# Optimization experiments

Hardware: AMD Instinct MI355X
Metric: run time of the kernel (lower is better)

The kernel has to match this reference:

```python
import jax, jax.numpy as jnp
import numpy as np

B, T, D = 4, 2048, 1024
DEPTH = 4
LEAF_DIM = 256
NUM_LEAVES = 2 ** DEPTH          # 16
NUM_NODES = NUM_LEAVES - 1       # 15


def _uniform(key, shape, scale):
    s = 1.0 / np.sqrt(scale)
    return jax.random.uniform(key, shape, minval=-s, maxval=s, dtype=jnp.float32)


def setup_inputs() -> dict:
    key = jax.random.key(0)
    ks = jax.random.split(key, 8)
    x = jax.random.normal(ks[0], (B, T, D), dtype=jnp.float32)
    # gate params: Dense(1) per internal node, level-order layout
    node_w = _uniform(ks[1], (NUM_NODES, D), D)
    node_b = _uniform(ks[2], (NUM_NODES,), D)
    # leaf MLP params: D -> LEAF_DIM -> D, stacked over leaves
    w1 = _uniform(ks[3], (NUM_LEAVES, D, LEAF_DIM), D)
    b1 = _uniform(ks[4], (NUM_LEAVES, LEAF_DIM), D)
    w2 = _uniform(ks[5], (NUM_LEAVES, LEAF_DIM, D), LEAF_DIM)
    b2 = _uniform(ks[6], (NUM_LEAVES, D), LEAF_DIM)
    return {"x": x, "node_w": node_w, "node_b": node_b,
            "w1": w1, "b1": b1, "w2": w2, "b2": b2, "training": 0}


def _leaf_probs(x, node_w, node_b, depth):
    # gate activations for all internal nodes at once: [B,T,NUM_NODES]
    c = jax.nn.sigmoid(jnp.einsum('btd,nd->btn', x, node_w) + node_b)
    probs = jnp.ones(c.shape[:-1] + (1,), dtype=c.dtype)
    for m in range(depth):
        start = 2 ** m - 1
        cl = c[..., start:start + 2 ** m]          # gates at level m: [B,T,2^m]
        # left child gets c, right child gets (1-c); interleave preserves
        # the recursion's n -> (2n, 2n+1) indexing
        probs = jnp.stack([probs * cl, probs * (1.0 - cl)], axis=-1)
        probs = probs.reshape(probs.shape[:-2] + (-1,))
    return probs                                   # [B,T,NUM_LEAVES]


def reference(x, node_w, node_b, w1, b1, w2, b2, training):
    num_leaves = w1.shape[0]
    depth = int(np.log2(num_leaves))
    probs = _leaf_probs(x, node_w, node_b, depth)          # [B,T,L]
    # all leaf MLP hidden layers as one batched GEMM
    h = jax.nn.relu(jnp.einsum('btd,ldh->btlh', x, w1) + b1)
    # weight hidden by leaf probability, then contract l and h together so the
    # [B,T,L,D] per-leaf output is never materialized
    h = h * probs[..., None]
    out = jnp.einsum('btlh,lhd->btd', h, w2)
    out = out + jnp.einsum('btl,ld->btd', probs, b2)
    return out
```

## Files before the change

kernel.cpp:

```cpp
#include <hip/hip_runtime.h>
#include <stdint.h>

typedef unsigned short ushort_t;
typedef __bf16 bf16x8 __attribute__((ext_vector_type(8)));
typedef float f32x4 __attribute__((ext_vector_type(4)));

#define M_TOK 8192
#define K1 1024
#define N1 4096
#define K2 4160
#define N2 1024

template <int V> struct ic { static constexpr int value = V; };

__device__ __forceinline__ ushort_t f2bf(float f) {
  union { float f; unsigned u; } v; v.f = f;
  unsigned u = v.u;
  u += 0x7FFFu + ((u >> 16) & 1u);
  return (ushort_t)(u >> 16);
}

__device__ __forceinline__ void gload16(const void* g, void* l) {
  __builtin_amdgcn_global_load_lds((__attribute__((address_space(1))) void*)g,
                                   (__attribute__((address_space(3))) void*)l,
                                   16, 0, 0);
}

__global__ __launch_bounds__(256) void k_prep(
    const float* __restrict__ x, const float* __restrict__ node_w,
    const float* __restrict__ node_b, const float* __restrict__ w1,
    const float* __restrict__ w2, const float* __restrict__ b2,
    ushort_t* __restrict__ xb, float* __restrict__ probs,
    ushort_t* __restrict__ w1t, ushort_t* __restrict__ w2t,
    ushort_t* __restrict__ hp) {
  __shared__ ushort_t tile[64][68];
  const int b = blockIdx.x;
  if (b < 1024) {
    const int tr = threadIdx.x >> 4, tc = (threadIdx.x & 15) * 4;
    const int l = b >> 6, rem = b & 63;
    const int kt = rem >> 2, ht = rem & 3;
    const float* in = w1 + (size_t)l * K1 * 256;
#pragma unroll
    for (int rr = 0; rr < 4; ++rr) {
      int r = tr + rr * 16;
      float4 v = *(const float4*)(in + (size_t)(kt * 64 + r) * 256 + ht * 64 + tc);
      tile[r][tc+0] = f2bf(v.x); tile[r][tc+1] = f2bf(v.y);
      tile[r][tc+2] = f2bf(v.z); tile[r][tc+3] = f2bf(v.w);
    }
    __syncthreads();
#pragma unroll
    for (int rr = 0; rr < 4; ++rr) {
      int oh = tr + rr * 16;
      ushort4 o;
      o.x = tile[tc+0][oh]; o.y = tile[tc+1][oh];
      o.z = tile[tc+2][oh]; o.w = tile[tc+3][oh];
      *(ushort4*)(w1t + (size_t)(l * 256 + ht * 64 + oh) * K1 + kt * 64 + tc) = o;
    }
  } else if (b < 2048) {
    const int tr = threadIdx.x >> 4, tc = (threadIdx.x & 15) * 4;
    const int bb = b - 1024;
    const int l = bb >> 6, rem = bb & 63;
    const int ht = rem >> 4, dt = rem & 15;
    const float* in = w2 + (size_t)l * 256 * N2;
#pragma unroll
    for (int rr = 0; rr < 4; ++rr) {
      int r = tr + rr * 16;
      float4 v = *(const float4*)(in + (size_t)(ht * 64 + r) * N2 + dt * 64 + tc);
      tile[r][tc+0] = f2bf(v.x); tile[r][tc+1] = f2bf(v.y);
      tile[r][tc+2] = f2bf(v.z); tile[r][tc+3] = f2bf(v.w);
    }
    __syncthreads();
#pragma unroll
    for (int rr = 0; rr < 4; ++rr) {
      int od = tr + rr * 16;
      ushort4 o;
      o.x = tile[tc+0][od]; o.y = tile[tc+1][od];
      o.z = tile[tc+2][od]; o.w = tile[tc+3][od];
      *(ushort4*)(w2t + (size_t)(dt * 64 + od) * K2 + l * 256 + ht * 64 + tc) = o;
    }
  } else if (b < 2304) {
    int tid = (b - 2048) * 256 + threadIdx.x;
    int d = tid >> 6, cc = tid & 63;
    float v = (cc < 16) ? b2[cc * N2 + d] : 0.f;
    w2t[(size_t)d * K2 + 4096 + cc] = f2bf(v);
  } else {
    const int wid = threadIdx.x >> 6, lane = threadIdx.x & 63;
    const int t = (b - 2304) * 4 + wid;
    const float* xr = x + (size_t)t * K1;
    float xv[16];
#pragma unroll
    for (int j = 0; j < 4; ++j) {
      float4 v = *(const float4*)(xr + j * 256 + lane * 4);
      xv[4*j+0] = v.x; xv[4*j+1] = v.y; xv[4*j+2] = v.z; xv[4*j+3] = v.w;
    }
    ushort_t* xbr = xb + (size_t)t * K1;
#pragma unroll
    for (int j = 0; j < 4; ++j) {
      ushort4 o;
      o.x = f2bf(xv[4*j+0]); o.y = f2bf(xv[4*j+1]);
      o.z = f2bf(xv[4*j+2]); o.w = f2bf(xv[4*j+3]);
      *(ushort4*)(xbr + j * 256 + lane * 4) = o;
    }
    float c[15];
#pragma unroll
    for (int n = 0; n < 15; ++n) {
      float s = 0.f;
      const float* wr = node_w + n * K1;
#pragma unroll
      for (int j = 0; j < 4; ++j) {
        float4 w = *(const float4*)(wr + j * 256 + lane * 4);
        s += xv[4*j+0]*w.x + xv[4*j+1]*w.y + xv[4*j+2]*w.z + xv[4*j+3]*w.w;
      }
#pragma unroll
      for (int off = 32; off > 0; off >>= 1) s += __shfl_xor(s, off);
      float z = s + node_b[n];
      c[n] = 1.f / (1.f + __expf(-z));
    }
    if (lane < 16) {
      float p = 1.f;
#pragma unroll
      for (int m = 0; m < 4; ++m) {
        int jm = lane >> (4 - m);
        int node = (1 << m) - 1 + jm;
        int bit = (lane >> (3 - m)) & 1;
        p *= bit ? (1.f - c[node]) : c[node];
      }
      probs[t * 16 + lane] = p;
      hp[(size_t)t * K2 + 4096 + lane] = f2bf(p);
    }
    if (lane < 48) hp[(size_t)t * K2 + 4112 + lane] = 0;
  }
}

template <int NT, int LDA, int LDB, int BN, int MODE>
__global__ __launch_bounds__(512, 2) void k_gemm8(
    const ushort_t* __restrict__ A, const ushort_t* __restrict__ Bt,
    const float* __restrict__ probs, const float* __restrict__ b1,
    ushort_t* __restrict__ hp, float* __restrict__ out, int ntn) {
  constexpr int BHR = BN / 2;
  constexpr int WN = (BN == 256) ? 4 : 2;
  constexpr int WM = 8 / WN;
  constexpr int FH = 128 / (WM * 16);
  constexpr int ABYTES = 128 * 128;
  constexpr int BBYTES = BHR * 128;
  constexpr int KEEP = 2 + 2 * (BHR / 64);

  extern __shared__ char lds[];
  const int tid = threadIdx.x;
  int bid = blockIdx.x;
  const int nwg = gridDim.x;
  bid = (bid & 7) * (nwg >> 3) + (bid >> 3);
  const int bm = bid / ntn, bn = bid % ntn;

  const int wid = tid >> 6, lane = tid & 63;
  const int widM = wid / WN, widN = wid % WN;
  const int wmBase = widM * (FH * 16);
  const int wn = widN * 64;
  const int lr = lane & 15, g = lane >> 4;

  const ushort_t* Ag = A + (size_t)bm * 256 * LDA;
  const ushort_t* Bg = Bt + (size_t)bn * BN * LDB;

  const int srow = tid >> 3;
  const int scol = ((tid & 7) << 4) ^ ((srow & 7) << 4);

  const char* pA = (const char*)(Ag + (size_t)srow * LDA) + scol;
  const char* pB = (const char*)(Bg + (size_t)srow * LDB) + scol;

  auto stageA = [&](int buf, int half, int kt) {
    const char* src = pA + (size_t)(half * 128) * (LDA * 2) + kt * 128;
    char* dst = lds + (buf * 2 + half) * ABYTES + tid * 16;
#pragma unroll
    for (int r = 0; r < 2; ++r)
      gload16(src + (size_t)(r * 64) * (LDA * 2), dst + r * 8192);
  };
  auto stageB = [&](int buf, int half, int kt) {
    const char* src = pB + (size_t)(half * BHR) * (LDB * 2) + kt * 128;
    char* dst = lds + 4 * ABYTES + (buf * 2 + half) * BBYTES + tid * 16;
#pragma unroll
    for (int r = 0; r < BHR / 64; ++r)
      gload16(src + (size_t)(r * 64) * (LDB * 2), dst + r * 8192);
  };
  auto rdA = [&](int buf, int half, int i, int kk) -> bf16x8 {
    int r = wmBase + i * 16 + lr;
    int off = r * 128 + (((kk * 4 + g) ^ (lr & 7)) << 4);
    return *(const bf16x8*)(lds + (buf * 2 + half) * ABYTES + off);
  };
  auto rdB = [&](int buf, int j, int kk) -> bf16x8 {
    int nr = wn + j * 16;
    int half = (nr >= BHR) ? 1 : 0;
    int r = (nr & (BHR - 1)) + lr;
    int off = r * 128 + (((kk * 4 + g) ^ (lr & 7)) << 4);
    return *(const bf16x8*)(lds + 4 * ABYTES + (buf * 2 + half) * BBYTES + off);
  };

  f32x4 acc[2 * FH][4];
#pragma unroll
  for (int i = 0; i < 2 * FH; ++i)
#pragma unroll
    for (int j = 0; j < 4; ++j) acc[i][j] = (f32x4){0.f, 0.f, 0.f, 0.f};

  stageA(0, 0, 0); stageA(0, 1, 0); stageB(0, 0, 0); stageB(0, 1, 0);
  stageA(1, 0, 1); stageB(1, 0, 1); stageB(1, 1, 1);
  if constexpr (KEEP == 6) asm volatile("s_waitcnt vmcnt(6)" ::: "memory");
  else                     asm volatile("s_waitcnt vmcnt(4)" ::: "memory");
  __builtin_amdgcn_sched_barrier(0);
  __builtin_amdgcn_s_barrier();
  __builtin_amdgcn_sched_barrier(0);

  auto body = [&](auto CURC, int kt) {
    constexpr int cur = decltype(CURC)::value;
    bf16x8 bfr[2][4];
    {
      bf16x8 a0[FH][2];
#pragma unroll
      for (int kk = 0; kk < 2; ++kk) {
#pragma unroll
        for (int i = 0; i < FH; ++i) a0[i][kk] = rdA(cur, 0, i, kk);
#pragma unroll
        for (int j = 0; j < 4; ++j) bfr[kk][j] = rdB(cur, j, kk);
      }
      if (kt + 1 < NT) stageA(cur ^ 1, 1, kt + 1);
      __builtin_amdgcn_s_setprio(1);
#pragma unroll
      for (int kk = 0; kk < 2; ++kk)
#pragma unroll
        for (int j = 0; j < 4; ++j)
#pragma unroll
          for (int i = 0; i < FH; ++i)
            acc[i][j] = __builtin_amdgcn_mfma_f32_16x16x32_bf16(
                a0[i][kk], bfr[kk][j], acc[i][j], 0, 0, 0);
      __builtin_amdgcn_s_setprio(0);
    }
    __builtin_amdgcn_s_barrier();
    __builtin_amdgcn_sched_barrier(0);
    {
      bf16x8 a1[FH][2];
#pragma unroll
      for (int kk = 0; kk < 2; ++kk)
#pragma unroll
        for (int i = 0; i < FH; ++i) a1[i][kk] = rdA(cur, 1, i, kk);
      if (kt + 2 < NT) {
        stageA(cur, 0, kt + 2);
        stageB(cur, 0, kt + 2);
        stageB(cur, 1, kt + 2);
      }
      __builtin_amdgcn_s_setprio(1);
#pragma unroll
      for (int kk = 0; kk < 2; ++kk)
#pragma unroll
        for (int j = 0; j < 4; ++j)
#pragma unroll
          for (int i = 0; i < FH; ++i)
            acc[FH + i][j] = __builtin_amdgcn_mfma_f32_16x16x32_bf16(
                a1[i][kk], bfr[kk][j], acc[FH + i][j], 0, 0, 0);
      __builtin_amdgcn_s_setprio(0);
    }
    if (kt + 2 < NT) {
      if constexpr (KEEP == 6) asm volatile("s_waitcnt vmcnt(6)" ::: "memory");
      else                     asm volatile("s_waitcnt vmcnt(4)" ::: "memory");
      __builtin_amdgcn_sched_barrier(0);
    } else if (kt + 1 < NT) {
      asm volatile("s_waitcnt vmcnt(0)" ::: "memory");
      __builtin_amdgcn_sched_barrier(0);
    }
    __builtin_amdgcn_s_barrier();
    __builtin_amdgcn_sched_barrier(0);
  };

  int kt = 0;
#pragma unroll 1
  for (int it = 0; it < NT / 2; ++it) {
    body(ic<0>{}, kt); ++kt;
    body(ic<1>{}, kt); ++kt;
  }
  if constexpr (NT & 1) body(ic<0>{}, kt);

  const int rowb = bm * 256 + wmBase + g * 4;
  const int colb = bn * BN + wn + lr;
  if (MODE == 0) {
    const int leaf = bn;
#pragma unroll
    for (int q = 0; q < 2; ++q)
#pragma unroll
      for (int i = 0; i < FH; ++i) {
        int rbase = rowb + q * 128 + i * 16;
        float pm[4];
#pragma unroll
        for (int rg = 0; rg < 4; ++rg)
          pm[rg] = probs[(size_t)(rbase + rg) * 16 + leaf];
#pragma unroll
        for (int j = 0; j < 4; ++j) {
          float bias = b1[colb + j * 16];
#pragma unroll
          for (int rg = 0; rg < 4; ++rg) {
            float v = acc[q * FH + i][j][rg] + bias;
            v = v > 0.f ? v : 0.f;
            v *= pm[rg];
            hp[(size_t)(rbase + rg) * K2 + colb + j * 16] = f2bf(v);
          }
        }
      }
  } else {
#pragma unroll
    for (int q = 0; q < 2; ++q)
#pragma unroll
      for (int i = 0; i < FH; ++i) {
        int rbase = rowb + q * 128 + i * 16;
#pragma unroll
        for (int j = 0; j < 4; ++j)
#pragma unroll
          for (int rg = 0; rg < 4; ++rg)
            out[(size_t)(rbase + rg) * N2 + colb + j * 16] = acc[q * FH + i][j][rg];
      }
  }
}

extern "C" void kernel_launch(void* const* d_in, const int* in_sizes, int n_in,
                              void* d_out, int out_size, void* d_ws, size_t ws_size,
                              hipStream_t stream) {
  const float* x      = (const float*)d_in[0];
  const float* node_w = (const float*)d_in[1];
  const float* node_b = (const float*)d_in[2];
  const float* w1     = (const float*)d_in[3];
  const float* b1     = (const float*)d_in[4];
  const float* w2     = (const float*)d_in[5];
  const float* b2     = (const float*)d_in[6];
  float* out = (float*)d_out;

  char* ws = (char*)d_ws;
  ushort_t* xb    = (ushort_t*)(ws);
  ushort_t* w1t   = (ushort_t*)(ws + 16777216);
  ushort_t* w2t   = (ushort_t*)(ws + 25165824);
  ushort_t* hp    = (ushort_t*)(ws + 33685504);
  float*    probs = (float*)   (ws + 101842944);

  k_prep<<<4352, 256, 0, stream>>>(x, node_w, node_b, w1, w2, b2,
                                   xb, probs, w1t, w2t, hp);
  k_gemm8<16, K1, K1, 256, 0><<<512, 512, 131072, stream>>>(
      xb, w1t, probs, b1, hp, nullptr, N1 / 256);
  k_gemm8<65, K2, K2, 128, 1><<<256, 512, 98304, stream>>>(
      hp, w2t, nullptr, nullptr, nullptr, out, N2 / 128);
}
```

Measured before the change: 169.0 us.

## Shrink GEMM tiles to 128 rows and K-step 32 for higher occupancy

The templated GEMM now uses a BM=128 row tile and a 32-element K step per stage, down from 256 rows and 64. Each single A buffer is loaded whole instead of in two halves, and the LDS swizzle is redone for 64-byte rows. LDS use drops to 48KB and 32KB per block, launch bounds allow 4 blocks per CU, and the grids double. Occupancy and wave count go up to hide latency better, at the cost of twice as many K iterations and barriers, less data reuse per tile and more global traffic.

```diff
diff --git a/kernel.cpp b/kernel.cpp
--- a/kernel.cpp
+++ b/kernel.cpp
@@ -132,18 +132,21 @@
   }
 }
 
-template <int NT, int LDA, int LDB, int BN, int MODE>
-__global__ __launch_bounds__(512, 2) void k_gemm8(
+template <int NT, int LDA, int LDB, int BM, int BN, int THREADS, int MODE>
+__global__ __launch_bounds__(THREADS, 4) void k_gemm(
     const ushort_t* __restrict__ A, const ushort_t* __restrict__ Bt,
     const float* __restrict__ probs, const float* __restrict__ b1,
     ushort_t* __restrict__ hp, float* __restrict__ out, int ntn) {
+  constexpr int NWAVE = THREADS / 64;
+  constexpr int WN = (BN == 256) ? 4 : 2;
+  constexpr int WM = NWAVE / WN;
+  constexpr int HA = BM / 2;
+  constexpr int FH = HA / (WM * 16);
   constexpr int BHR = BN / 2;
-  constexpr int WN = (BN == 256) ? 4 : 2;
-  constexpr int WM = 8 / WN;
-  constexpr int FH = 128 / (WM * 16);
-  constexpr int ABYTES = 128 * 128;
-  constexpr int BBYTES = BHR * 128;
-  constexpr int KEEP = 2 + 2 * (BHR / 64);
+  constexpr int ATILE = BM * 64;
+  constexpr int BBYTES = BHR * 64;
+  constexpr int BOFF = 2 * ATILE;
+  constexpr int AR = (BM * 64) / (THREADS * 16);
 
   extern __shared__ char lds[];
   const int tid = threadIdx.x;
@@ -157,41 +160,35 @@
   const int wmBase = widM * (FH * 16);
   const int wn = widN * 64;
   const int lr = lane & 15, g = lane >> 4;
-
-  const ushort_t* Ag = A + (size_t)bm * 256 * LDA;
+  const int swz = (g ^ ((lr >> 1) & 3)) << 4;
+
+  const ushort_t* Ag = A + (size_t)bm * BM * LDA;
   const ushort_t* Bg = Bt + (size_t)bn * BN * LDB;
 
-  const int srow = tid >> 3;
-  const int scol = ((tid & 7) << 4) ^ ((srow & 7) << 4);
-
-  const char* pA = (const char*)(Ag + (size_t)srow * LDA) + scol;
-  const char* pB = (const char*)(Bg + (size_t)srow * LDB) + scol;
-
-  auto stageA = [&](int buf, int half, int kt) {
-    const char* src = pA + (size_t)(half * 128) * (LDA * 2) + kt * 128;
-    char* dst = lds + (buf * 2 + half) * ABYTES + tid * 16;
-#pragma unroll
-    for (int r = 0; r < 2; ++r)
-      gload16(src + (size_t)(r * 64) * (LDA * 2), dst + r * 8192);
+  auto stageA = [&](int buf, int kt) {
+#pragma unroll
+    for (int r = 0; r < AR; ++r) {
+      int srow = (tid >> 2) + r * (THREADS / 4);
+      int scol = (((tid & 3) ^ ((srow >> 1) & 3)) << 4);
+      gload16((const char*)(Ag + (size_t)srow * LDA) + kt * 64 + scol,
+              lds + buf * ATILE + r * (THREADS * 16) + tid * 16);
+    }
   };
   auto stageB = [&](int buf, int half, int kt) {
-    const char* src = pB + (size_t)(half * BHR) * (LDB * 2) + kt * 128;
-    char* dst = lds + 4 * ABYTES + (buf * 2 + half) * BBYTES + tid * 16;
-#pragma unroll
-    for (int r = 0; r < BHR / 64; ++r)
-      gload16(src + (size_t)(r * 64) * (LDB * 2), dst + r * 8192);
-  };
-  auto rdA = [&](int buf, int half, int i, int kk) -> bf16x8 {
-    int r = wmBase + i * 16 + lr;
-    int off = r * 128 + (((kk * 4 + g) ^ (lr & 7)) << 4);
-    return *(const bf16x8*)(lds + (buf * 2 + half) * ABYTES + off);
-  };
-  auto rdB = [&](int buf, int j, int kk) -> bf16x8 {
+    int srow = tid >> 2;
+    int scol = (((tid & 3) ^ ((srow >> 1) & 3)) << 4);
+    gload16((const char*)(Bg + (size_t)(half * BHR + srow) * LDB) + kt * 64 + scol,
+            lds + BOFF + (buf * 2 + half) * BBYTES + tid * 16);
+  };
+  auto rdA = [&](int buf, int half, int i) -> bf16x8 {
+    int row = half * HA + wmBase + i * 16 + lr;
+    return *(const bf16x8*)(lds + buf * ATILE + row * 64 + swz);
+  };
+  auto rdB = [&](int buf, int j) -> bf16x8 {
     int nr = wn + j * 16;
     int half = (nr >= BHR) ? 1 : 0;
     int r = (nr & (BHR - 1)) + lr;
-    int off = r * 128 + (((kk * 4 + g) ^ (lr & 7)) << 4);
-    return *(const bf16x8*)(lds + 4 * ABYTES + (buf * 2 + half) * BBYTES + off);
+    return *(const bf16x8*)(lds + BOFF + (buf * 2 + half) * BBYTES + r * 64 + swz);
   };
 
   f32x4 acc[2 * FH][4];
@@ -200,65 +197,50 @@
 #pragma unroll
     for (int j = 0; j < 4; ++j) acc[i][j] = (f32x4){0.f, 0.f, 0.f, 0.f};
 
-  stageA(0, 0, 0); stageA(0, 1, 0); stageB(0, 0, 0); stageB(0, 1, 0);
-  stageA(1, 0, 1); stageB(1, 0, 1); stageB(1, 1, 1);
-  if constexpr (KEEP == 6) asm volatile("s_waitcnt vmcnt(6)" ::: "memory");
-  else                     asm volatile("s_waitcnt vmcnt(4)" ::: "memory");
+  stageA(0, 0); stageB(0, 0, 0); stageB(0, 1, 0);
+  stageB(1, 0, 1); stageB(1, 1, 1);
+  asm volatile("s_waitcnt vmcnt(2)" ::: "memory");
   __builtin_amdgcn_sched_barrier(0);
   __builtin_amdgcn_s_barrier();
   __builtin_amdgcn_sched_barrier(0);
 
   auto body = [&](auto CURC, int kt) {
     constexpr int cur = decltype(CURC)::value;
-    bf16x8 bfr[2][4];
+    bf16x8 bfr[4];
     {
-      bf16x8 a0[FH][2];
-#pragma unroll
-      for (int kk = 0; kk < 2; ++kk) {
-#pragma unroll
-        for (int i = 0; i < FH; ++i) a0[i][kk] = rdA(cur, 0, i, kk);
-#pragma unroll
-        for (int j = 0; j < 4; ++j) bfr[kk][j] = rdB(cur, j, kk);
-      }
-      if (kt + 1 < NT) stageA(cur ^ 1, 1, kt + 1);
+      bf16x8 a0[FH];
+#pragma unroll
+      for (int i = 0; i < FH; ++i) a0[i] = rdA(cur, 0, i);
+#pragma unroll
+      for (int j = 0; j < 4; ++j) bfr[j] = rdB(cur, j);
+      if (kt + 1 < NT) stageA(cur ^ 1, kt + 1);
       __builtin_amdgcn_s_setprio(1);
 #pragma unroll
-      for (int kk = 0; kk < 2; ++kk)
-#pragma unroll
-        for (int j = 0; j < 4; ++j)
-#pragma unroll
-          for (int i = 0; i < FH; ++i)
-            acc[i][j] = __builtin_amdgcn_mfma_f32_16x16x32_bf16(
-                a0[i][kk], bfr[kk][j], acc[i][j], 0, 0, 0);
+      for (int j = 0; j < 4; ++j)
+#pragma unroll
+        for (int i = 0; i < FH; ++i)
+          acc[i][j] = __builtin_amdgcn_mfma_f32_16x16x32_bf16(
+              a0[i], bfr[j], acc[i][j], 0, 0, 0);
       __builtin_amdgcn_s_setprio(0);
     }
     __builtin_amdgcn_s_barrier();
     __builtin_amdgcn_sched_barrier(0);
     {
-      bf16x8 a1[FH][2];
-#pragma unroll
-      for (int kk = 0; kk < 2; ++kk)
-#pragma unroll
-        for (int i = 0; i < FH; ++i) a1[i][kk] = rdA(cur, 1, i, kk);
-      if (kt + 2 < NT) {
-        stageA(cur, 0, kt + 2);
-        stageB(cur, 0, kt + 2);
-        stageB(cur, 1, kt + 2);
-      }
+      bf16x8 a1[FH];
+#pragma unroll
+      for (int i = 0; i < FH; ++i) a1[i] = rdA(cur, 1, i);
+      if (kt + 2 < NT) { stageB(cur, 0, kt + 2); stageB(cur, 1, kt + 2); }
       __builtin_amdgcn_s_setprio(1);
 #pragma unroll
-      for (int kk = 0; kk < 2; ++kk)
-#pragma unroll
-        for (int j = 0; j < 4; ++j)
-#pragma unroll
-          for (int i = 0; i < FH; ++i)
-            acc[FH + i][j] = __builtin_amdgcn_mfma_f32_16x16x32_bf16(
-                a1[i][kk], bfr[kk][j], acc[FH + i][j], 0, 0, 0);
+      for (int j = 0; j < 4; ++j)
+#pragma unroll
+        for (int i = 0; i < FH; ++i)
+          acc[FH + i][j] = __builtin_amdgcn_mfma_f32_16x16x32_bf16(
+              a1[i], bfr[j], acc[FH + i][j], 0, 0, 0);
       __builtin_amdgcn_s_setprio(0);
     }
     if (kt + 2 < NT) {
-      if constexpr (KEEP == 6) asm volatile("s_waitcnt vmcnt(6)" ::: "memory");
-      else                     asm volatile("s_waitcnt vmcnt(4)" ::: "memory");
+      asm volatile("s_waitcnt vmcnt(2)" ::: "memory");
       __builtin_amdgcn_sched_barrier(0);
     } else if (kt + 1 < NT) {
       asm volatile("s_waitcnt vmcnt(0)" ::: "memory");
@@ -274,9 +256,8 @@
     body(ic<0>{}, kt); ++kt;
     body(ic<1>{}, kt); ++kt;
   }
-  if constexpr (NT & 1) body(ic<0>{}, kt);
-
-  const int rowb = bm * 256 + wmBase + g * 4;
+
+  const int rowb = bm * BM + wmBase + g * 4;
   const int colb = bn * BN + wn + lr;
   if (MODE == 0) {
     const int leaf = bn;
@@ -284,7 +265,7 @@
     for (int q = 0; q < 2; ++q)
 #pragma unroll
       for (int i = 0; i < FH; ++i) {
-        int rbase = rowb + q * 128 + i * 16;
+        int rbase = rowb + q * HA + i * 16;
         float pm[4];
 #pragma unroll
         for (int rg = 0; rg < 4; ++rg)
@@ -306,7 +287,7 @@
     for (int q = 0; q < 2; ++q)
 #pragma unroll
       for (int i = 0; i < FH; ++i) {
-        int rbase = rowb + q * 128 + i * 16;
+        int rbase = rowb + q * HA + i * 16;
 #pragma unroll
         for (int j = 0; j < 4; ++j)
 #pragma unroll
@@ -337,8 +318,8 @@
 
   k_prep<<<4352, 256, 0, stream>>>(x, node_w, node_b, w1, w2, b2,
                                    xb, probs, w1t, w2t, hp);
-  k_gemm8<16, K1, K1, 256, 0><<<512, 512, 131072, stream>>>(
+  k_gemm<32, K1, K1, 128, 256, 512, 0><<<1024, 512, 49152, stream>>>(
       xb, w1t, probs, b1, hp, nullptr, N1 / 256);
-  k_gemm8<65, K2, K2, 128, 1><<<256, 512, 98304, stream>>>(
+  k_gemm<130, K2, K2, 128, 128, 256, 1><<<512, 256, 32768, stream>>>(
       hp, w2t, nullptr, nullptr, nullptr, out, N2 / 128);
 }
```

Result: slower. 188.5 us (+11.5%).

## Replace second GEMM with kernel loading A directly to registers, B via LDS

Applied to the files above, without the earlier changes.

Adds a new GEMM kernel for the second (hidden x W2) product that keeps only the B tile in double-buffered LDS (32KB), while each wave loads its A fragments straight from global memory into registers with a ping-pong prefetch. Tiles are 256x128 over the same 256-block grid, with an XCD-aware block remap and setprio around the MFMA section. The aim is to cut LDS footprint and LDS traffic for A so two workgroups fit per CU. The cost is uncoalesced, unshared per-wave global loads of A and higher register pressure.

```diff
diff --git a/kernel.cpp b/kernel.cpp
--- a/kernel.cpp
+++ b/kernel.cpp
@@ -316,6 +316,116 @@
   }
 }
 
+template <int NT>
+__global__ __launch_bounds__(512, 2) void k_gemm2d(
+    const ushort_t* __restrict__ A, const ushort_t* __restrict__ Bt,
+    float* __restrict__ out, int ntn) {
+  constexpr int BB = 128 * 128;
+  extern __shared__ char lds[];
+  const int tid = threadIdx.x;
+  int bid = blockIdx.x;
+  const int nwg = gridDim.x;
+  bid = (bid & 7) * (nwg >> 3) + (bid >> 3);
+  const int bm = bid / ntn, bn = bid % ntn;
+
+  const int wid = tid >> 6, lane = tid & 63;
+  const int widM = wid >> 1, widN = wid & 1;
+  const int lr = lane & 15, g = lane >> 4;
+
+  const ushort_t* Ag = A + (size_t)(bm * 256 + widM * 64) * K2;
+  const ushort_t* Bg = Bt + (size_t)bn * 128 * K2;
+
+  auto stageB = [&](int buf, int kt) {
+#pragma unroll
+    for (int r = 0; r < 2; ++r) {
+      int s = tid + r * 512;
+      int row = s >> 3;
+      int c16 = (s & 7) ^ (row & 7);
+      gload16((const char*)(Bg + (size_t)row * K2) + kt * 128 + (c16 << 4),
+              lds + buf * BB + s * 16);
+    }
+  };
+  auto rdB = [&](int buf, int nj, int kk) -> bf16x8 {
+    int nr = widN * 64 + nj * 16 + lr;
+    return *(const bf16x8*)(lds + buf * BB + nr * 128 +
+                            (((kk * 4 + g) ^ (nr & 7)) << 4));
+  };
+  auto ldA = [&](bf16x8 (&dst)[4][2], int kt) {
+#pragma unroll
+    for (int fi = 0; fi < 4; ++fi)
+#pragma unroll
+      for (int kk = 0; kk < 2; ++kk)
+        dst[fi][kk] = *(const bf16x8*)(
+            (const char*)(Ag + (size_t)(fi * 16 + lr) * K2) +
+            kt * 128 + kk * 64 + g * 16);
+  };
+
+  f32x4 acc[4][4];
+#pragma unroll
+  for (int i = 0; i < 4; ++i)
+#pragma unroll
+    for (int j = 0; j < 4; ++j) acc[i][j] = (f32x4){0.f, 0.f, 0.f, 0.f};
+
+  bf16x8 aP[4][2], aQ[4][2];
+
+  stageB(0, 0);
+  __builtin_amdgcn_sched_barrier(0);
+  ldA(aP, 0);
+  asm volatile("s_waitcnt vmcnt(8)" ::: "memory");
+  __builtin_amdgcn_sched_barrier(0);
+  __builtin_amdgcn_s_barrier();
+  __builtin_amdgcn_sched_barrier(0);
+
+  auto body = [&](auto PC, int kt, bf16x8 (&aCur)[4][2], bf16x8 (&aNxt)[4][2]) {
+    constexpr int P = decltype(PC)::value;
+    if (kt + 1 < NT) stageB(P ^ 1, kt + 1);
+    __builtin_amdgcn_sched_barrier(0);
+    if (kt + 1 < NT) ldA(aNxt, kt + 1);
+    __builtin_amdgcn_sched_barrier(0);
+    bf16x8 bfr[4][2];
+#pragma unroll
+    for (int nj = 0; nj < 4; ++nj)
+#pragma unroll
+      for (int kk = 0; kk < 2; ++kk) bfr[nj][kk] = rdB(P, nj, kk);
+    __builtin_amdgcn_s_setprio(1);
+#pragma unroll
+    for (int kk = 0; kk < 2; ++kk)
+#pragma unroll
+      for (int nj = 0; nj < 4; ++nj)
+#pragma unroll
+        for (int mi = 0; mi < 4; ++mi)
+          acc[mi][nj] = __builtin_amdgcn_mfma_f32_16x16x32_bf16(
+              aCur[mi][kk], bfr[nj][kk], acc[mi][nj], 0, 0, 0);
+    __builtin_amdgcn_s_setprio(0);
+    if (kt + 1 < NT) {
+      asm volatile("s_waitcnt vmcnt(8)" ::: "memory");
+      __builtin_amdgcn_sched_barrier(0);
+      __builtin_amdgcn_s_barrier();
+      __builtin_amdgcn_sched_barrier(0);
+    }
+  };
+
+  int kt = 0;
+#pragma unroll 1
+  for (int it = 0; it < NT / 2; ++it) {
+    body(ic<0>{}, kt, aP, aQ); ++kt;
+    body(ic<1>{}, kt, aQ, aP); ++kt;
+  }
+  if constexpr (NT & 1) body(ic<0>{}, kt, aP, aQ);
+
+  const int rowb = bm * 256 + widM * 64 + g * 4;
+  const int colb = bn * 128 + widN * 64 + lr;
+#pragma unroll
+  for (int mi = 0; mi < 4; ++mi) {
+    int rbase = rowb + mi * 16;
+#pragma unroll
+    for (int nj = 0; nj < 4; ++nj)
+#pragma unroll
+      for (int rg = 0; rg < 4; ++rg)
+        out[(size_t)(rbase + rg) * N2 + colb + nj * 16] = acc[mi][nj][rg];
+  }
+}
+
 extern "C" void kernel_launch(void* const* d_in, const int* in_sizes, int n_in,
                               void* d_out, int out_size, void* d_ws, size_t ws_size,
                               hipStream_t stream) {
@@ -339,6 +449,5 @@
                                    xb, probs, w1t, w2t, hp);
   k_gemm8<16, K1, K1, 256, 0><<<512, 512, 131072, stream>>>(
       xb, w1t, probs, b1, hp, nullptr, N1 / 256);
-  k_gemm8<65, K2, K2, 128, 1><<<256, 512, 98304, stream>>>(
-      hp, w2t, nullptr, nullptr, nullptr, out, N2 / 128);
-}
+  k_gemm2d<65><<<256, 512, 32768, stream>>>(hp, w2t, out, N2 / 128);
+}
```

Result: slower. 252.4 us (+49.3%).
